# Optimization experiments

Measured on AMD Instinct MI355X. Metric: run time of the kernel, lower is better.

## Reference

```python
import jax, jax.numpy as jnp
import numpy as np

EPS = 1e-5

def rmsnorm(x, w, eps=EPS):
    # torch-style RMSNorm: x / rms(x) * weight
    return x * jax.lax.rsqrt(jnp.mean(x * x, axis=-1, keepdims=True) + eps) * w

def setup_inputs() -> dict:
    key = jax.random.key(0)
    k1, k2 = jax.random.split(key)
    B, T, D, Q, K = 8, 1024, 1024, 8, 4096
    d = D // Q
    x = jax.random.normal(k1, (B, T, D), dtype=jnp.float32)
    codebooks = jax.random.normal(k2, (Q, K, d), dtype=jnp.float32)
    input_norm_w = jnp.ones((D,), dtype=jnp.float32)
    output_norm_w = jnp.ones((D,), dtype=jnp.float32)
    return {"x": x, "codebooks": codebooks,
            "input_norm_w": input_norm_w, "output_norm_w": output_norm_w}

def reference(x, codebooks, input_norm_w, output_norm_w):
    B, T, D = x.shape
    Q, K, d = codebooks.shape
    xn = rmsnorm(x, input_norm_w)
    xq = xn.reshape(B, T, Q, d)  # split hidden into Q sub-vectors
    # squared euclidean distances (argmin equal to cdist argmin)
    x2 = jnp.sum(xq * xq, axis=-1, keepdims=True)          # [B,T,Q,1]
    c2 = jnp.sum(codebooks * codebooks, axis=-1)           # [Q,K]
    xc = jnp.einsum('btqd,qkd->btqk', xq, codebooks)       # [B,T,Q,K]
    d2 = x2 - 2.0 * xc + c2[None, None]                    # [B,T,Q,K]
    idx = jnp.argmin(d2, axis=-1)                          # [B,T,Q] int
    # gather nearest code per quantizer: equivalent of stacked embedding lookups
    quant = codebooks[jnp.arange(Q)[None, None, :], idx]   # [B,T,Q,d]
    quant = quant.reshape(B, T, D)
    out = rmsnorm(quant, output_norm_w)
    return out, idx
```

## Files before the change

### kernel.cpp

```cpp
#include <hip/hip_runtime.h>
#include <math.h>
#include <float.h>

#define Q_     8
#define K_     4096
#define dd_    128
#define D_     1024
#define ROWS   8192
#define NCHUNK 64
#define TAU    0.02f

typedef __attribute__((ext_vector_type(8))) _Float16 f16x8;
typedef __attribute__((ext_vector_type(4))) float f32x4;
typedef __attribute__((ext_vector_type(4))) unsigned int u32x4;

typedef const __attribute__((address_space(1))) unsigned int* gas_p;
typedef __attribute__((address_space(3))) unsigned int* las_p;

__device__ inline unsigned f2u(float x) { union { float f; unsigned u; } v; v.f = x; return v.u; }
__device__ inline float u2f(unsigned x) { union { unsigned u; float f; } v; v.u = x; return v.f; }
__device__ inline unsigned short f2h(float x) {
    union { _Float16 h; unsigned short u; } v; v.h = (_Float16)x; return v.u;
}
__device__ inline unsigned umin_(unsigned a, unsigned b) { return a < b ? a : b; }
__device__ inline unsigned umax_(unsigned a, unsigned b) { return a > b ? a : b; }
__device__ inline unsigned fflip(float x) {
    unsigned u = f2u(x);
    return (u & 0x80000000u) ? ~u : (u | 0x80000000u);
}
__device__ inline unsigned long long shfl_xor_u64(unsigned long long v, int m) {
    unsigned lo = (unsigned)v, hi = (unsigned)(v >> 32);
    lo = __shfl_xor(lo, m, 64);
    hi = __shfl_xor(hi, m, 64);
    return ((unsigned long long)hi << 32) | lo;
}
__device__ inline unsigned dec_k(unsigned v, int e) {
    unsigned tg = v & 0x7Fu;
    return ((tg >> 1) << 6) | (((unsigned)e >> 4) << 5) | ((tg & 1u) << 4) | ((unsigned)e & 15u);
}

__global__ void k_prep(const float* __restrict__ cb, const float* __restrict__ x,
                       const float* __restrict__ w, float* __restrict__ xn,
                       unsigned short* __restrict__ panels, float* __restrict__ c2h,
                       float* __restrict__ x2h, int* __restrict__ cntF, int* __restrict__ cntS) {
    const int bid = blockIdx.x, t = threadIdx.x;
    if (bid == 0 && t == 0) { *cntF = 0; *cntS = 0; }
    if (bid < NCHUNK * Q_) {
        int c = bid & 63, q = bid >> 6;
        const float* src = cb + ((size_t)q * K_ + c * 64) * dd_;
        unsigned short* dst = panels + (size_t)(q * NCHUNK + c) * 8192;
        #pragma unroll
        for (int i = 0; i < 4; i++) {
            int sid = i * 256 + t;
            int n = sid >> 4, j = sid & 15;
            const float* sp = src + n * dd_ + j * 8;
            f32x4 v0 = *(const f32x4*)sp;
            f32x4 v1 = *(const f32x4*)(sp + 4);
            float xs[8] = {v0.x, v0.y, v0.z, v0.w, v1.x, v1.y, v1.z, v1.w};
            unsigned short hb[8];
            float ss = 0.0f;
            #pragma unroll
            for (int e = 0; e < 8; e++) {
                float xv = -xs[e];
                ss = fmaf(xv, xv, ss);
                hb[e] = f2h(xv);
            }
            int slot = j ^ (n & 15);
            u32x4 H;
            H.x = (unsigned)hb[0] | ((unsigned)hb[1] << 16);
            H.y = (unsigned)hb[2] | ((unsigned)hb[3] << 16);
            H.z = (unsigned)hb[4] | ((unsigned)hb[5] << 16);
            H.w = (unsigned)hb[6] | ((unsigned)hb[7] << 16);
            *(u32x4*)&dst[(n * 16 + slot) * 8] = H;
            ss += __shfl_xor(ss, 1, 64);
            ss += __shfl_xor(ss, 2, 64);
            ss += __shfl_xor(ss, 4, 64);
            ss += __shfl_xor(ss, 8, 64);
            if (j == 0) c2h[q * K_ + c * 64 + n] = 0.5f * ss;
        }
    } else {
        int row = bid - NCHUNK * Q_;
        const float4 v = *(const float4*)(x + (size_t)row * D_ + t * 4);
        float ss = v.x * v.x + v.y * v.y + v.z * v.z + v.w * v.w;
        #pragma unroll
        for (int o = 32; o > 0; o >>= 1) ss += __shfl_xor(ss, o, 64);
        __shared__ float acc[4];
        if ((t & 63) == 0) acc[t >> 6] = ss;
        __syncthreads();
        float tot = (acc[0] + acc[1]) + (acc[2] + acc[3]);
        float sc  = 1.0f / sqrtf(tot * (1.0f / D_) + 1e-5f);
        const float4 wv = *(const float4*)(w + t * 4);
        float4 o;
        o.x = v.x * sc * wv.x; o.y = v.y * sc * wv.y;
        o.z = v.z * sc * wv.z; o.w = v.w * sc * wv.w;
        *(float4*)(xn + (size_t)row * D_ + t * 4) = o;
        float so = o.x * o.x + o.y * o.y + o.z * o.z + o.w * o.w;
        so += __shfl_xor(so, 1, 64);
        so += __shfl_xor(so, 2, 64);
        so += __shfl_xor(so, 4, 64);
        so += __shfl_xor(so, 8, 64);
        so += __shfl_xor(so, 16, 64);
        if ((t & 31) == 0) x2h[row * Q_ + (t >> 5)] = 0.5f * so;
    }
}

#define STAGE(CN) do {                                                                   \
    const char* src_ = (const char*)(panels + panq + (size_t)(CN) * 8192);               \
    char* stg_ = smem + ((CN) & 1) * 16384;                                              \
    _Pragma("unroll")                                                                    \
    for (int i_ = 0; i_ < 4; i_++) {                                                     \
        int boff_ = i_ * 4096 + t * 16;                                                  \
        __builtin_amdgcn_global_load_lds((gas_p)(src_ + boff_), (las_p)(stg_ + boff_),   \
                                         16, 0, 0);                                      \
    }                                                                                    \
} while (0)

__launch_bounds__(256, 4)
__global__ void k_dist(const float* __restrict__ xn, const unsigned short* __restrict__ panels,
                       const float* __restrict__ c2h, const float* __restrict__ x2h,
                       int* __restrict__ idxi, float* __restrict__ idxf,
                       int* __restrict__ listF, int* __restrict__ cntF,
                       int* __restrict__ srl, int* __restrict__ cntS,
                       unsigned long long* __restrict__ resc) {
    __shared__ char smem[32768];

    const int t    = threadIdx.x;
    const int lane = t & 63, wave = t >> 6;
    const int wm = wave >> 1, wn = wave & 1;
    const int col = lane & 15, quad = lane >> 4;
    const int q = blockIdx.y;
    const int row0 = blockIdx.x * 64;

    f16x8 ah[2][4], al[2][4];
    #pragma unroll
    for (int mt = 0; mt < 2; mt++) {
        #pragma unroll
        for (int kt = 0; kt < 4; kt++) {
            const float* ap = xn + (size_t)(row0 + wm * 32 + mt * 16 + col) * D_
                              + q * dd_ + kt * 32 + quad * 8;
            f32x4 v0 = *(const f32x4*)ap;
            f32x4 v1 = *(const f32x4*)(ap + 4);
            #pragma unroll
            for (int e = 0; e < 8; e++) {
                float xv = (e < 4) ? v0[e] : v1[e - 4];
                _Float16 h = (_Float16)xv;
                float r = xv - (float)h;
                ah[mt][kt][e] = h;
                al[mt][kt][e] = (_Float16)r;
            }
        }
    }

    f32x4 x2v[2];
    #pragma unroll
    for (int mt = 0; mt < 2; mt++)
        #pragma unroll
        for (int r = 0; r < 4; r++)
            x2v[mt][r] = x2h[(size_t)(row0 + wm * 32 + mt * 16 + quad * 4 + r) * Q_ + q];

    unsigned m1[8], m2[8];
    #pragma unroll
    for (int i = 0; i < 8; i++) { m1[i] = 0xFFFFFFFFu; m2[i] = 0xFFFFFFFFu; }

    const size_t panq = (size_t)q * NCHUNK * 8192;
    const float* c2hq = c2h + q * K_;

    STAGE(0);
    float ch0 = c2hq[wn * 32 + col];
    float ch1 = c2hq[wn * 32 + col + 16];

    for (int c = 0; c < NCHUNK; c++) {
        __syncthreads();
        if (c + 1 < NCHUNK) STAGE(c + 1);
        float ch0n = 0.0f, ch1n = 0.0f;
        if (c + 1 < NCHUNK) {
            ch0n = c2hq[(c + 1) * 64 + wn * 32 + col];
            ch1n = c2hq[(c + 1) * 64 + wn * 32 + col + 16];
        }
        const char* cbuf = smem + (c & 1) * 16384;

        f32x4 acc[2][2];
        #pragma unroll
        for (int mt = 0; mt < 2; mt++) {
            acc[mt][0] = x2v[mt] + ch0;
            acc[mt][1] = x2v[mt] + ch1;
        }

        #pragma unroll
        for (int kt = 0; kt < 4; kt++) {
            const int sw = ((quad + kt * 4) ^ col) * 16;
            const int a0 = (wn * 32 + col) * 256 + sw;
            const int a1 = a0 + 4096;
            f16x8 b0 = *(const f16x8*)(cbuf + a0);
            f16x8 b1 = *(const f16x8*)(cbuf + a1);
            #pragma unroll
            for (int mt = 0; mt < 2; mt++) {
                acc[mt][0] = __builtin_amdgcn_mfma_f32_16x16x32_f16(ah[mt][kt], b0, acc[mt][0], 0, 0, 0);
                acc[mt][0] = __builtin_amdgcn_mfma_f32_16x16x32_f16(al[mt][kt], b0, acc[mt][0], 0, 0, 0);
                acc[mt][1] = __builtin_amdgcn_mfma_f32_16x16x32_f16(ah[mt][kt], b1, acc[mt][1], 0, 0, 0);
                acc[mt][1] = __builtin_amdgcn_mfma_f32_16x16x32_f16(al[mt][kt], b1, acc[mt][1], 0, 0, 0);
            }
        }

        const unsigned tg0 = (unsigned)(c << 1), tg1 = tg0 | 1u;
        #pragma unroll
        for (int mt = 0; mt < 2; mt++) {
            #pragma unroll
            for (int r = 0; r < 4; r++) {
                const int sl = mt * 4 + r;
                unsigned p0 = (f2u(acc[mt][0][r]) & 0xFFFFFF80u) | tg0;
                unsigned p1 = (f2u(acc[mt][1][r]) & 0xFFFFFF80u) | tg1;
                unsigned pmin = umin_(p0, p1), pmax = umax_(p0, p1);
                m2[sl] = umin_(umin_(m2[sl], umax_(m1[sl], pmin)), pmax);
                m1[sl] = umin_(m1[sl], pmin);
            }
        }
        ch0 = ch0n; ch1 = ch1n;
    }

    __syncthreads();
    unsigned* rm1 = (unsigned*)smem;
    unsigned* rm2 = (unsigned*)(smem + 8448);
    #pragma unroll
    for (int mt = 0; mt < 2; mt++) {
        #pragma unroll
        for (int r = 0; r < 4; r++) {
            int sl = mt * 4 + r;
            int row_l = wm * 32 + mt * 16 + quad * 4 + r;
            int e = wn * 16 + col;
            rm1[row_l * 33 + e] = m1[sl];
            rm2[row_l * 33 + e] = m2[sl];
        }
    }
    __syncthreads();
    if (t < 64) {
        unsigned b1 = 0xFFFFFFFFu;
        int be = 0;
        for (int e = 0; e < 32; e++) {
            unsigned v1 = rm1[t * 33 + e];
            if (v1 < b1) { b1 = v1; be = e; }
        }
        float thr = u2f(b1 & 0xFFFFFF80u) + TAU;
        int ns = 0, fb = 0;
        unsigned long long candpack = 0;
        for (int e = 0; e < 32; e++) {
            if (u2f(rm2[t * 33 + e] & 0xFFFFFF80u) < thr) fb = 1;
            if (e != be) {
                unsigned v1 = rm1[t * 33 + e];
                if (u2f(v1 & 0xFFFFFF80u) < thr) {
                    if (ns < 5) candpack |= (unsigned long long)dec_k(v1, e) << (12 * ns);
                    ns++;
                }
            }
        }
        if (ns > 5) fb = 1;
        unsigned k1 = dec_k(b1, be);
        int item = (row0 + t) * Q_ + q;
        idxi[item] = (int)k1;
        idxf[item] = (float)k1;
        if (fb) {
            resc[item] = 0xFFFFFFFFFFFFFFFFull;
            int p = atomicAdd(cntF, 1);
            listF[p] = item;
        } else if (ns > 0) {
            int p = atomicAdd(cntS, 1);
            int* e8 = srl + (size_t)p * 8;
            e8[0] = item; e8[1] = ns + 1; e8[2] = (int)k1;
            for (int i = 0; i < ns; i++)
                e8[3 + i] = (int)((candpack >> (12 * i)) & 0xFFFu);
        }
    }
}

__global__ void k_rescue(const float* __restrict__ xn, const float* __restrict__ cb,
                         const float* __restrict__ c2h, const int* __restrict__ listF,
                         const int* __restrict__ cntF, const int* __restrict__ srl,
                         const int* __restrict__ cntS,
                         unsigned long long* __restrict__ resc,
                         int* __restrict__ idxi, float* __restrict__ idxf) {
    __shared__ float xq[dd_];
    __shared__ unsigned long long kshare[8];
    const int t = threadIdx.x;
    if (blockIdx.x < 2048) {
        const int n = *cntF;
        const int seg = blockIdx.x & 7;
        for (int ii = blockIdx.x >> 3; ii < n; ii += 256) {
            __syncthreads();
            int item = listF[ii];
            int rg = item >> 3, q = item & 7;
            if (t < dd_) xq[t] = xn[(size_t)rg * D_ + q * dd_ + t];
            __syncthreads();
            unsigned long long best = 0xFFFFFFFFFFFFFFFFull;
            #pragma unroll
            for (int i = 0; i < 2; i++) {
                int k = seg * 512 + i * 256 + t;
                const float* cp = cb + ((size_t)q * K_ + k) * dd_;
                float dot = 0.0f;
                #pragma unroll 8
                for (int d = 0; d < dd_; d += 4) {
                    f32x4 cv = *(const f32x4*)(cp + d);
                    dot = fmaf(cv.x, xq[d],     dot);
                    dot = fmaf(cv.y, xq[d + 1], dot);
                    dot = fmaf(cv.z, xq[d + 2], dot);
                    dot = fmaf(cv.w, xq[d + 3], dot);
                }
                float s = c2h[q * K_ + k] - dot;
                unsigned long long key = ((unsigned long long)fflip(s) << 32) | (unsigned)k;
                best = best < key ? best : key;
            }
            #pragma unroll
            for (int o = 32; o > 0; o >>= 1) {
                unsigned long long other = shfl_xor_u64(best, o);
                best = best < other ? best : other;
            }
            if ((t & 63) == 0) kshare[t >> 6] = best;
            __syncthreads();
            if (t == 0) {
                unsigned long long b = kshare[0];
                b = b < kshare[1] ? b : kshare[1];
                b = b < kshare[2] ? b : kshare[2];
                b = b < kshare[3] ? b : kshare[3];
                atomicMin(&resc[item], b);
            }
        }
    } else {
        const int n = *cntS;
        for (int ii = (int)blockIdx.x - 2048; ii < n; ii += 2048) {
            __syncthreads();
            const int* e = srl + (size_t)ii * 8;
            int item = e[0], nc = e[1];
            int rg = item >> 3, q = item & 7;
            if (t < dd_) xq[t] = xn[(size_t)rg * D_ + q * dd_ + t];
            __syncthreads();
            int g = t >> 5, l = t & 31;
            unsigned long long key = 0xFFFFFFFFFFFFFFFFull;
            if (g < nc) {
                int k = e[2 + g];
                const float* cp = cb + ((size_t)q * K_ + k) * dd_ + l * 4;
                f32x4 cv = *(const f32x4*)cp;
                float dot = cv.x * xq[l * 4]     + cv.y * xq[l * 4 + 1]
                          + cv.z * xq[l * 4 + 2] + cv.w * xq[l * 4 + 3];
                dot += __shfl_xor(dot, 16, 64);
                dot += __shfl_xor(dot, 8, 64);
                dot += __shfl_xor(dot, 4, 64);
                dot += __shfl_xor(dot, 2, 64);
                dot += __shfl_xor(dot, 1, 64);
                float s = c2h[q * K_ + k] - dot;
                key = ((unsigned long long)fflip(s) << 32) | (unsigned)k;
            }
            if (l == 0) kshare[g] = key;
            __syncthreads();
            if (t == 0) {
                unsigned long long b = kshare[0];
                #pragma unroll
                for (int gg = 1; gg < 8; gg++) b = b < kshare[gg] ? b : kshare[gg];
                int k = (int)(unsigned)(b & 0xFFFFFFFFull);
                idxi[item] = k;
                idxf[item] = (float)k;
            }
        }
    }
}

__global__ void k_fin(const int* __restrict__ listF, const int* __restrict__ cntF,
                      const unsigned long long* __restrict__ resc,
                      int* __restrict__ idxi, float* __restrict__ idxf) {
    const int n = *cntF;
    for (int i = blockIdx.x * blockDim.x + threadIdx.x; i < n; i += gridDim.x * blockDim.x) {
        int item = listF[i];
        int k = (int)(unsigned)(resc[item] & 0xFFFFFFFFull);
        idxi[item] = k;
        idxf[item] = (float)k;
    }
}

__global__ void k_out(const float* __restrict__ cb, const int* __restrict__ idx_i,
                      const float* __restrict__ w, float* __restrict__ out) {
    int row = blockIdx.x;
    int t   = threadIdx.x;
    __shared__ int   sidx[Q_];
    __shared__ float acc[4];
    if (t < Q_) sidx[t] = idx_i[row * Q_ + t];
    __syncthreads();
    int col = t * 4;
    int q   = col >> 7;
    int dc  = col & 127;
    const float4 v = *(const float4*)(cb + ((size_t)q * K_ + sidx[q]) * dd_ + dc);
    float ss = v.x * v.x + v.y * v.y + v.z * v.z + v.w * v.w;
    #pragma unroll
    for (int o = 32; o > 0; o >>= 1) ss += __shfl_xor(ss, o, 64);
    if ((t & 63) == 0) acc[t >> 6] = ss;
    __syncthreads();
    float tot = (acc[0] + acc[1]) + (acc[2] + acc[3]);
    float sc  = 1.0f / sqrtf(tot * (1.0f / D_) + 1e-5f);
    const float4 wv = *(const float4*)(w + col);
    float4 o;
    o.x = v.x * sc * wv.x; o.y = v.y * sc * wv.y;
    o.z = v.z * sc * wv.z; o.w = v.w * sc * wv.w;
    *(float4*)(out + (size_t)row * D_ + col) = o;
}

extern "C" void kernel_launch(void* const* d_in, const int* in_sizes, int n_in,
                              void* d_out, int out_size, void* d_ws, size_t ws_size,
                              hipStream_t stream) {
    const float* x     = (const float*)d_in[0];
    const float* cb    = (const float*)d_in[1];
    const float* w_in  = (const float*)d_in[2];
    const float* w_out = (const float*)d_in[3];

    float* out  = (float*)d_out;
    float* idxf = out + (size_t)ROWS * D_;

    unsigned short* panels = (unsigned short*)d_ws;
    float* c2h  = (float*)((char*)d_ws + (8u << 20));
    float* x2h  = c2h + Q_ * K_;
    unsigned long long* resc = (unsigned long long*)(x2h + (size_t)ROWS * Q_);
    int*   idxi = (int*)(resc + (size_t)ROWS * Q_);
    int*   listF = idxi + ROWS * Q_;
    int*   srl  = listF + ROWS * Q_;
    int*   cntF = srl + (size_t)ROWS * Q_ * 8;
    int*   cntS = cntF + 1;

    k_prep  <<<dim3(NCHUNK * Q_ + ROWS), 256, 0, stream>>>(cb, x, w_in, out, panels, c2h, x2h, cntF, cntS);
    k_dist  <<<dim3(ROWS / 64, Q_),      256, 0, stream>>>(out, panels, c2h, x2h, idxi, idxf, listF, cntF, srl, cntS, resc);
    k_rescue<<<dim3(4096),               256, 0, stream>>>(out, cb, c2h, listF, cntF, srl, cntS, resc, idxi, idxf);
    k_fin   <<<dim3(64),                 256, 0, stream>>>(listF, cntF, resc, idxi, idxf);
    k_out   <<<dim3(ROWS),               256, 0, stream>>>(cb, idxi, w_out, out);
}
```

Before: 249.1 us.

## Drop split-fp16 low MFMA pass, track top-3 per lane, fuse finalize into output

Distances are now computed with a single fp16 MFMA per tile instead of the hi/lo split, halving the matrix work in the distance kernel. To cover the larger rounding error, the candidate margin TAU is doubled and each lane tracks a third-smallest value, so the second-best per lane also becomes a candidate and the third triggers fallback. The separate finalize kernel is removed: a per-item fallback flag lets the output kernel pick up rescued indices directly. The cost is more candidates and fallbacks going to the exact rescue pass, plus extra registers and shared memory for the third minimum.

```diff
diff --git a/kernel.cpp b/kernel.cpp
--- a/kernel.cpp
+++ b/kernel.cpp
@@ -8,7 +8,7 @@
 #define D_     1024
 #define ROWS   8192
 #define NCHUNK 64
-#define TAU    0.02f
+#define TAU    0.04f
 
 typedef __attribute__((ext_vector_type(8))) _Float16 f16x8;
 typedef __attribute__((ext_vector_type(4))) float f32x4;
@@ -121,7 +121,8 @@
                        int* __restrict__ idxi, float* __restrict__ idxf,
                        int* __restrict__ listF, int* __restrict__ cntF,
                        int* __restrict__ srl, int* __restrict__ cntS,
-                       unsigned long long* __restrict__ resc) {
+                       unsigned long long* __restrict__ resc,
+                       unsigned char* __restrict__ fbm) {
     __shared__ char smem[32768];
 
     const int t    = threadIdx.x;
@@ -131,7 +132,7 @@
     const int q = blockIdx.y;
     const int row0 = blockIdx.x * 64;
 
-    f16x8 ah[2][4], al[2][4];
+    f16x8 ah[2][4];
     #pragma unroll
     for (int mt = 0; mt < 2; mt++) {
         #pragma unroll
@@ -143,10 +144,7 @@
             #pragma unroll
             for (int e = 0; e < 8; e++) {
                 float xv = (e < 4) ? v0[e] : v1[e - 4];
-                _Float16 h = (_Float16)xv;
-                float r = xv - (float)h;
-                ah[mt][kt][e] = h;
-                al[mt][kt][e] = (_Float16)r;
+                ah[mt][kt][e] = (_Float16)xv;
             }
         }
     }
@@ -158,9 +156,9 @@
         for (int r = 0; r < 4; r++)
             x2v[mt][r] = x2h[(size_t)(row0 + wm * 32 + mt * 16 + quad * 4 + r) * Q_ + q];
 
-    unsigned m1[8], m2[8];
+    unsigned m1[8], m2[8], m3[8];
     #pragma unroll
-    for (int i = 0; i < 8; i++) { m1[i] = 0xFFFFFFFFu; m2[i] = 0xFFFFFFFFu; }
+    for (int i = 0; i < 8; i++) { m1[i] = 0xFFFFFFFFu; m2[i] = 0xFFFFFFFFu; m3[i] = 0xFFFFFFFFu; }
 
     const size_t panq = (size_t)q * NCHUNK * 8192;
     const float* c2hq = c2h + q * K_;
@@ -196,9 +194,7 @@
             #pragma unroll
             for (int mt = 0; mt < 2; mt++) {
                 acc[mt][0] = __builtin_amdgcn_mfma_f32_16x16x32_f16(ah[mt][kt], b0, acc[mt][0], 0, 0, 0);
-                acc[mt][0] = __builtin_amdgcn_mfma_f32_16x16x32_f16(al[mt][kt], b0, acc[mt][0], 0, 0, 0);
                 acc[mt][1] = __builtin_amdgcn_mfma_f32_16x16x32_f16(ah[mt][kt], b1, acc[mt][1], 0, 0, 0);
-                acc[mt][1] = __builtin_amdgcn_mfma_f32_16x16x32_f16(al[mt][kt], b1, acc[mt][1], 0, 0, 0);
             }
         }
 
@@ -211,8 +207,13 @@
                 unsigned p0 = (f2u(acc[mt][0][r]) & 0xFFFFFF80u) | tg0;
                 unsigned p1 = (f2u(acc[mt][1][r]) & 0xFFFFFF80u) | tg1;
                 unsigned pmin = umin_(p0, p1), pmax = umax_(p0, p1);
-                m2[sl] = umin_(umin_(m2[sl], umax_(m1[sl], pmin)), pmax);
+                unsigned a1m = umax_(m1[sl], pmin);
+                unsigned a2m = umin_(m2[sl], pmax);
+                unsigned a4m = umax_(m2[sl], pmax);
                 m1[sl] = umin_(m1[sl], pmin);
+                m2[sl] = umin_(a1m, a2m);
+                unsigned a3m = umax_(a1m, a2m);
+                m3[sl] = umin_(umin_(a3m, a4m), m3[sl]);
             }
         }
         ch0 = ch0n; ch1 = ch1n;
@@ -221,6 +222,7 @@
     __syncthreads();
     unsigned* rm1 = (unsigned*)smem;
     unsigned* rm2 = (unsigned*)(smem + 8448);
+    unsigned* rm3 = (unsigned*)(smem + 16896);
     #pragma unroll
     for (int mt = 0; mt < 2; mt++) {
         #pragma unroll
@@ -230,6 +232,7 @@
             int e = wn * 16 + col;
             rm1[row_l * 33 + e] = m1[sl];
             rm2[row_l * 33 + e] = m2[sl];
+            rm3[row_l * 33 + e] = m3[sl];
         }
     }
     __syncthreads();
@@ -244,13 +247,17 @@
         int ns = 0, fb = 0;
         unsigned long long candpack = 0;
         for (int e = 0; e < 32; e++) {
-            if (u2f(rm2[t * 33 + e] & 0xFFFFFF80u) < thr) fb = 1;
-            if (e != be) {
-                unsigned v1 = rm1[t * 33 + e];
-                if (u2f(v1 & 0xFFFFFF80u) < thr) {
-                    if (ns < 5) candpack |= (unsigned long long)dec_k(v1, e) << (12 * ns);
-                    ns++;
-                }
+            unsigned v1 = rm1[t * 33 + e];
+            unsigned v2 = rm2[t * 33 + e];
+            unsigned v3 = rm3[t * 33 + e];
+            if (u2f(v3 & 0xFFFFFF80u) < thr) fb = 1;
+            if (e != be && u2f(v1 & 0xFFFFFF80u) < thr) {
+                if (ns < 5) candpack |= (unsigned long long)dec_k(v1, e) << (12 * ns);
+                ns++;
+            }
+            if (u2f(v2 & 0xFFFFFF80u) < thr) {
+                if (ns < 5) candpack |= (unsigned long long)dec_k(v2, e) << (12 * ns);
+                ns++;
             }
         }
         if (ns > 5) fb = 1;
@@ -258,6 +265,7 @@
         int item = (row0 + t) * Q_ + q;
         idxi[item] = (int)k1;
         idxf[item] = (float)k1;
+        fbm[item] = (unsigned char)fb;
         if (fb) {
             resc[item] = 0xFFFFFFFFFFFFFFFFull;
             int p = atomicAdd(cntF, 1);
@@ -362,25 +370,24 @@
     }
 }
 
-__global__ void k_fin(const int* __restrict__ listF, const int* __restrict__ cntF,
+__global__ void k_out(const float* __restrict__ cb, const int* __restrict__ idx_i,
                       const unsigned long long* __restrict__ resc,
-                      int* __restrict__ idxi, float* __restrict__ idxf) {
-    const int n = *cntF;
-    for (int i = blockIdx.x * blockDim.x + threadIdx.x; i < n; i += gridDim.x * blockDim.x) {
-        int item = listF[i];
-        int k = (int)(unsigned)(resc[item] & 0xFFFFFFFFull);
-        idxi[item] = k;
-        idxf[item] = (float)k;
-    }
-}
-
-__global__ void k_out(const float* __restrict__ cb, const int* __restrict__ idx_i,
-                      const float* __restrict__ w, float* __restrict__ out) {
+                      const unsigned char* __restrict__ fbm,
+                      const float* __restrict__ w, float* __restrict__ out,
+                      float* __restrict__ idxf) {
     int row = blockIdx.x;
     int t   = threadIdx.x;
     __shared__ int   sidx[Q_];
     __shared__ float acc[4];
-    if (t < Q_) sidx[t] = idx_i[row * Q_ + t];
+    if (t < Q_) {
+        int item = row * Q_ + t;
+        int k = idx_i[item];
+        if (fbm[item]) {
+            k = (int)(unsigned)(resc[item] & 0xFFFFFFFFull);
+            idxf[item] = (float)k;
+        }
+        sidx[t] = k;
+    }
     __syncthreads();
     int col = t * 4;
     int q   = col >> 7;
@@ -418,12 +425,12 @@
     int*   idxi = (int*)(resc + (size_t)ROWS * Q_);
     int*   listF = idxi + ROWS * Q_;
     int*   srl  = listF + ROWS * Q_;
-    int*   cntF = srl + (size_t)ROWS * Q_ * 8;
+    unsigned char* fbm = (unsigned char*)(srl + (size_t)ROWS * Q_ * 8);
+    int*   cntF = (int*)(fbm + ROWS * Q_);
     int*   cntS = cntF + 1;
 
     k_prep  <<<dim3(NCHUNK * Q_ + ROWS), 256, 0, stream>>>(cb, x, w_in, out, panels, c2h, x2h, cntF, cntS);
-    k_dist  <<<dim3(ROWS / 64, Q_),      256, 0, stream>>>(out, panels, c2h, x2h, idxi, idxf, listF, cntF, srl, cntS, resc);
+    k_dist  <<<dim3(ROWS / 64, Q_),      256, 0, stream>>>(out, panels, c2h, x2h, idxi, idxf, listF, cntF, srl, cntS, resc, fbm);
     k_rescue<<<dim3(4096),               256, 0, stream>>>(out, cb, c2h, listF, cntF, srl, cntS, resc, idxi, idxf);
-    k_fin   <<<dim3(64),                 256, 0, stream>>>(listF, cntF, resc, idxi, idxf);
-    k_out   <<<dim3(ROWS),               256, 0, stream>>>(cb, idxi, w_out, out);
-}
+    k_out   <<<dim3(ROWS),               256, 0, stream>>>(cb, idxi, resc, fbm, w_out, out, idxf);
+}
```

Result: faster. 217.0 us (-12.9%).
